# Performance work log

Measured on AMD Instinct MI355X. Metric: run time of the kernel, lower is better.

Reference implementation:

```python
import jax, jax.numpy as jnp
import numpy as np

C = 8      # num_channels
H = 512    # dim_hidden
B, S = 32, 1024
EPS = 1e-5


def _layernorm(x, gamma, beta):
    mu = jnp.mean(x, axis=-1, keepdims=True)
    var = jnp.var(x, axis=-1, keepdims=True)
    return (x - mu) * jax.lax.rsqrt(var + EPS) * gamma + beta


def setup_inputs() -> dict:
    key = jax.random.key(0)
    ks = jax.random.split(key, 7)
    x = jax.random.normal(ks[0], (C, B, S, 1), dtype=jnp.float32)
    # per-channel Linear(1,H): torch weight [H,1] -> stacked as [C,H]
    enc_w = jax.random.normal(ks[1], (C, H), dtype=jnp.float32) / jnp.sqrt(1.0)
    enc_b = jax.random.normal(ks[2], (C, H), dtype=jnp.float32) * 0.02
    enc_gamma = jnp.ones((C, H), dtype=jnp.float32)
    enc_beta = jnp.zeros((C, H), dtype=jnp.float32)
    # modulator Linear(C*H -> H): torch weight [H, C*H]
    mod_w = jax.random.normal(ks[3], (H, C * H), dtype=jnp.float32) / jnp.sqrt(C * H)
    mod_b = jax.random.normal(ks[4], (H,), dtype=jnp.float32) * 0.02
    mod_gamma = jnp.ones((H,), dtype=jnp.float32)
    mod_beta = jnp.zeros((H,), dtype=jnp.float32)
    return {
        "x": x,
        "enc_w": enc_w, "enc_b": enc_b,
        "enc_gamma": enc_gamma, "enc_beta": enc_beta,
        "mod_w": mod_w, "mod_b": mod_b,
        "mod_gamma": mod_gamma, "mod_beta": mod_beta,
    }


def reference(x, enc_w, enc_b, enc_gamma, enc_beta, mod_w, mod_b, mod_gamma, mod_beta):
    # per-channel Linear(1,H): h[c,b,s,:] = x[c,b,s,0]*enc_w[c] + enc_b[c]
    h = x * enc_w[:, None, None, :] + enc_b[:, None, None, :]      # [C,B,S,H]
    h = _layernorm(h, enc_gamma[:, None, None, :], enc_beta[:, None, None, :])
    h = jax.nn.gelu(h, approximate=False)
    # concat along last dim in channel order -> [B,S,C*H]
    h = jnp.transpose(h, (1, 2, 0, 3)).reshape(B, S, C * H)
    # channel modulator: Linear + LayerNorm + GELU
    y = jnp.einsum("bsk,hk->bsh", h, mod_w) + mod_b                # [B,S,H]
    y = _layernorm(y, mod_gamma, mod_beta)
    return jax.nn.gelu(y, approximate=False)
```

## Files before the change

kernel.cpp:

```cpp
#include <hip/hip_runtime.h>
#include <hip/hip_bf16.h>
#include <math.h>

#define C_CH 8
#define H_DIM 512
#define BS 32768
#define K_DIM 4096
#define EPS 1e-5f

#define TM 64
#define TK 32
#define NKT (K_DIM / TK)
#define TMTK (TM * TK)

typedef __bf16 bf16x8 __attribute__((ext_vector_type(8)));
typedef __bf16 bf16x4 __attribute__((ext_vector_type(4)));
typedef float  floatx4 __attribute__((ext_vector_type(4)));

__device__ __forceinline__ float gelu_fast(float v) {
    float x2 = v * fmaf(v * v, 0.102943215f, 2.30220815f);
    float e = __builtin_amdgcn_exp2f(-x2);
    return v * __builtin_amdgcn_rcpf(1.0f + e);
}

__global__ __launch_bounds__(256) void prep_kernel(
    const float* __restrict__ w, __bf16* __restrict__ o,
    const float* __restrict__ enc_w, const float* __restrict__ enc_b,
    const float* __restrict__ enc_gamma,
    float* __restrict__ Wf, float* __restrict__ Bf, float* __restrict__ st)
{
    __shared__ float red[4][5];
    if (blockIdx.x < 1024) {
        int gtid  = blockIdx.x * 256 + threadIdx.x;
        int lane  = gtid & 63;
        int chunk = gtid >> 6;
        int kt    = chunk >> 5;
        int ntile = chunk & 31;
        int col   = ntile * 16 + (lane & 15);
        int k     = kt * 32 + (lane >> 4) * 8;
        const float* src = w + (size_t)col * K_DIM + k;
        float4 a = *(const float4*)src;
        float4 b = *(const float4*)(src + 4);
        bf16x8 h;
        h[0] = (__bf16)a.x; h[1] = (__bf16)a.y; h[2] = (__bf16)a.z; h[3] = (__bf16)a.w;
        h[4] = (__bf16)b.x; h[5] = (__bf16)b.y; h[6] = (__bf16)b.z; h[7] = (__bf16)b.w;
        *(bf16x8*)(o + (size_t)gtid * 8) = h;
    } else {
        const int c = blockIdx.x - 1024;
        const int t = threadIdx.x;
        const float* wp = enc_w + c * H_DIM;
        const float* bp = enc_b + c * H_DIM;
        const float* gp = enc_gamma + c * H_DIM;
        float w0 = wp[t], w1 = wp[t + 256];
        float b0 = bp[t], b1 = bp[t + 256];
        float sw  = w0 + w1;
        float sb  = b0 + b1;
        float sww = fmaf(w0, w0, w1 * w1);
        float sbb = fmaf(b0, b0, b1 * b1);
        float swb = fmaf(w0, b0, w1 * b1);
        #pragma unroll
        for (int off = 32; off; off >>= 1) {
            sw  += __shfl_xor(sw,  off);
            sb  += __shfl_xor(sb,  off);
            sww += __shfl_xor(sww, off);
            sbb += __shfl_xor(sbb, off);
            swb += __shfl_xor(swb, off);
        }
        int wv = t >> 6, ln = t & 63;
        if (ln == 0) {
            red[wv][0] = sw;  red[wv][1] = sb;  red[wv][2] = sww;
            red[wv][3] = sbb; red[wv][4] = swb;
        }
        __syncthreads();
        float tsw  = red[0][0] + red[1][0] + red[2][0] + red[3][0];
        float tsb  = red[0][1] + red[1][1] + red[2][1] + red[3][1];
        float tsww = red[0][2] + red[1][2] + red[2][2] + red[3][2];
        float tsbb = red[0][3] + red[1][3] + red[2][3] + red[3][3];
        float tswb = red[0][4] + red[1][4] + red[2][4] + red[3][4];
        const float inv = 1.0f / (float)H_DIM;
        float mw = tsw * inv, mb = tsb * inv;
        if (t == 0) {
            st[c * 4 + 0] = tsww * inv - mw * mw;
            st[c * 4 + 1] = 2.0f * (tswb * inv - mw * mb);
            st[c * 4 + 2] = tsbb * inv - mb * mb;
        }
        float g0 = gp[t], g1 = gp[t + 256];
        Wf[c * H_DIM + t]       = g0 * (w0 - mw);
        Wf[c * H_DIM + t + 256] = g1 * (w1 - mw);
        Bf[c * H_DIM + t]       = g0 * (b0 - mb);
        Bf[c * H_DIM + t + 256] = g1 * (b1 - mb);
    }
}

template <int USE_WS>
__global__ __launch_bounds__(512, 4) void fused_gemm_kernel(
    const float* __restrict__ x,
    const float* __restrict__ enc_w,
    const float* __restrict__ enc_b,
    const float* __restrict__ enc_gamma,
    const float* __restrict__ enc_beta,
    const float* __restrict__ mod_w,
    const __bf16* __restrict__ Wb,
    const float* __restrict__ Wf,
    const float* __restrict__ Bf,
    const float* __restrict__ st,
    const float* __restrict__ mod_b,
    const float* __restrict__ mod_gamma,
    const float* __restrict__ mod_beta,
    float* __restrict__ out)
{
    __shared__ float stats[C_CH][5];
    __shared__ float pS[C_CH][TM];
    __shared__ float qS[C_CH][TM];
    __shared__ float rS[C_CH][TM];
    __shared__ __align__(16) __bf16 Als[2 * 4 * TMTK];
    __shared__ float redS[TM][8];
    __shared__ float redQ[TM][8];
    __shared__ float muS[TM];
    __shared__ float invS[TM];

    const int tid  = threadIdx.x;
    const int wave = tid >> 6;
    const int lane = tid & 63;
    const int row0 = blockIdx.x * TM;

    if (USE_WS) {
        int c = wave;
        int m = lane;
        float xv = x[c * BS + row0 + m];
        float vw = st[c * 4 + 0], cwb2 = st[c * 4 + 1], vb = st[c * 4 + 2];
        float q = rsqrtf(fmaf(xv, fmaf(xv, vw, cwb2), vb) + EPS);
        pS[c][m] = xv * q;
        qS[c][m] = q;
    } else {
        {
            const int c = wave;
            float sw = 0.f, sb = 0.f, sww = 0.f, sbb = 0.f, swb = 0.f;
            for (int j = lane; j < H_DIM; j += 64) {
                float w = enc_w[c * H_DIM + j];
                float b = enc_b[c * H_DIM + j];
                sw += w; sb += b;
                sww = fmaf(w, w, sww);
                sbb = fmaf(b, b, sbb);
                swb = fmaf(w, b, swb);
            }
            #pragma unroll
            for (int off = 32; off; off >>= 1) {
                sw  += __shfl_xor(sw,  off);
                sb  += __shfl_xor(sb,  off);
                sww += __shfl_xor(sww, off);
                sbb += __shfl_xor(sbb, off);
                swb += __shfl_xor(swb, off);
            }
            if (lane == 0) {
                const float inv = 1.0f / (float)H_DIM;
                float mw = sw * inv, mb = sb * inv;
                stats[c][0] = mw;
                stats[c][1] = mb;
                stats[c][2] = sww * inv - mw * mw;
                stats[c][3] = sbb * inv - mb * mb;
                stats[c][4] = swb * inv - mw * mb;
            }
        }
        __syncthreads();
        {
            int c = wave;
            int m = lane;
            float xv = x[c * BS + row0 + m];
            float mw = stats[c][0], mb = stats[c][1];
            float vw = stats[c][2], vb = stats[c][3], cwb = stats[c][4];
            float var = fmaf(xv, fmaf(xv, vw, 2.0f * cwb), vb);
            float q = rsqrtf(var + EPS);
            float p = xv * q;
            pS[c][m] = p;
            qS[c][m] = q;
            rS[c][m] = -fmaf(p, mw, q * mb);
        }
    }
    __syncthreads();

    const int wn = wave;
    const int lr = lane & 15;
    const int lq = lane >> 4;

    const int arow  = tid >> 3;
    const int akq   = (tid >> 1) & 3;
    const int ahalf = tid & 1;
    const int wchunk = arow * 4 + (akq ^ ((arow >> 1) & 3));

    floatx4 acc[4][4];
    #pragma unroll
    for (int i = 0; i < 4; ++i)
        #pragma unroll
        for (int j = 0; j < 4; ++j)
            acc[i][j] = (floatx4){0.f, 0.f, 0.f, 0.f};

    auto stageA2 = [&](int ktn, __bf16* dst, float p, float q) {
        const int j0 = ktn * TK + akq * 8 + ahalf * 4;
        float4 w = *(const float4*)(Wf + j0);
        float4 b = *(const float4*)(Bf + j0);
        float4 e = *(const float4*)(enc_beta + j0);
        float fw[4] = {w.x, w.y, w.z, w.w};
        float fb[4] = {b.x, b.y, b.z, b.w};
        float fe[4] = {e.x, e.y, e.z, e.w};
        bf16x4 hv;
        #pragma unroll
        for (int i = 0; i < 4; ++i) {
            float v = fmaf(p, fw[i], fmaf(q, fb[i], fe[i]));
            hv[i] = (__bf16)gelu_fast(v);
        }
        *(bf16x4*)(dst + wchunk * 8 + ahalf * 4) = hv;
    };

    auto stageA_legacy = [&](int ktn, __bf16* dst) {
        const int k0 = ktn * TK;
        const int c  = k0 >> 9;
        const int j0 = c * H_DIM + (k0 & (H_DIM - 1)) + akq * 8 + ahalf * 4;
        float p = pS[c][arow], q = qS[c][arow], r = rS[c][arow];
        float4 w = *(const float4*)(enc_w + j0);
        float4 b = *(const float4*)(enc_b + j0);
        float4 g = *(const float4*)(enc_gamma + j0);
        float4 e = *(const float4*)(enc_beta + j0);
        float fw[4] = {w.x, w.y, w.z, w.w};
        float fb[4] = {b.x, b.y, b.z, b.w};
        float fg[4] = {g.x, g.y, g.z, g.w};
        float fe[4] = {e.x, e.y, e.z, e.w};
        bf16x4 hv;
        #pragma unroll
        for (int i = 0; i < 4; ++i) {
            float t = fmaf(p, fw[i], fmaf(q, fb[i], r));
            float v = fmaf(t, fg[i], fe[i]);
            hv[i] = (__bf16)gelu_fast(v);
        }
        *(bf16x4*)(dst + wchunk * 8 + ahalf * 4) = hv;
    };

    const __bf16* baseB = Wb + ((size_t)(wn * 4) * 64 + lane) * 8;
    auto loadB = [&](int ktn, int half, bf16x8* dst) {
        if (USE_WS) {
            const __bf16* bp = baseB + ktn * 16384 + half * 1024;
            dst[0] = *(const bf16x8*)(bp);
            dst[1] = *(const bf16x8*)(bp + 512);
        } else {
            const int kk = ktn * 32 + lq * 8;
            #pragma unroll
            for (int nt = 0; nt < 2; ++nt) {
                int col = wn * 64 + (half * 2 + nt) * 16 + lr;
                const float* src = mod_w + (size_t)col * K_DIM + kk;
                float4 a = *(const float4*)src;
                float4 b = *(const float4*)(src + 4);
                bf16x8 h;
                h[0] = (__bf16)a.x; h[1] = (__bf16)a.y; h[2] = (__bf16)a.z; h[3] = (__bf16)a.w;
                h[4] = (__bf16)b.x; h[5] = (__bf16)b.y; h[6] = (__bf16)b.z; h[7] = (__bf16)b.w;
                dst[nt] = h;
            }
        }
    };

    bf16x8 bfrP[2], bfrQ[2];
    loadB(0, 0, bfrP);
    if (USE_WS) {
        float p0 = pS[0][arow], q0 = qS[0][arow];
        #pragma unroll
        for (int sub = 0; sub < 4; ++sub)
            stageA2(sub, Als + sub * TMTK, p0, q0);
    } else {
        #pragma unroll
        for (int sub = 0; sub < 4; ++sub)
            stageA_legacy(sub, Als + sub * TMTK);
    }
    __syncthreads();

    for (int g = 0; g < NKT / 4; ++g) {
        const __bf16* cur = Als + (g & 1) * (4 * TMTK);
        __bf16*       nxt = Als + ((g + 1) & 1) * (4 * TMTK);
        const bool haveNext = (g + 1 < NKT / 4);

        float pC = 0.f, qC = 0.f;
        if (USE_WS && haveNext) {
            const int cn = (g + 1) >> 2;
            pC = pS[cn][arow];
            qC = qS[cn][arow];
        }

        #pragma unroll
        for (int sub = 0; sub < 4; ++sub) {
            const int kt = g * 4 + sub;

            loadB(kt, 1, bfrQ);

            if (haveNext) {
                if (USE_WS) stageA2(kt + 4, nxt + sub * TMTK, pC, qC);
                else        stageA_legacy(kt + 4, nxt + sub * TMTK);
            }

            const __bf16* Acur = cur + sub * TMTK;
            bf16x8 af[4];
            #pragma unroll
            for (int mt = 0; mt < 4; ++mt) {
                int row = mt * 16 + lr;
                int chunk = row * 4 + (lq ^ ((row >> 1) & 3));
                af[mt] = *(const bf16x8*)(Acur + chunk * 8);
            }

            #pragma unroll
            for (int mt = 0; mt < 4; ++mt)
                #pragma unroll
                for (int nt = 0; nt < 2; ++nt)
                    acc[mt][nt] = __builtin_amdgcn_mfma_f32_16x16x32_bf16(
                        af[mt], bfrP[nt], acc[mt][nt], 0, 0, 0);

            if (kt + 1 < NKT) loadB(kt + 1, 0, bfrP);

            #pragma unroll
            for (int mt = 0; mt < 4; ++mt)
                #pragma unroll
                for (int nt = 0; nt < 2; ++nt)
                    acc[mt][nt + 2] = __builtin_amdgcn_mfma_f32_16x16x32_bf16(
                        af[mt], bfrQ[nt], acc[mt][nt + 2], 0, 0, 0);
        }
        __syncthreads();
    }

    float mbv[4], gv[4], bev[4];
    #pragma unroll
    for (int nt = 0; nt < 4; ++nt) {
        int col = wn * 64 + nt * 16 + lr;
        mbv[nt] = mod_b[col];
        gv[nt]  = mod_gamma[col];
        bev[nt] = mod_beta[col];
    }
    #pragma unroll
    for (int mt = 0; mt < 4; ++mt)
        #pragma unroll
        for (int nt = 0; nt < 4; ++nt)
            #pragma unroll
            for (int r = 0; r < 4; ++r)
                acc[mt][nt][r] += mbv[nt];

    #pragma unroll
    for (int mt = 0; mt < 4; ++mt) {
        #pragma unroll
        for (int r = 0; r < 4; ++r) {
            float s = 0.f, ss = 0.f;
            #pragma unroll
            for (int nt = 0; nt < 4; ++nt) {
                float y = acc[mt][nt][r];
                s += y;
                ss = fmaf(y, y, ss);
            }
            #pragma unroll
            for (int off = 1; off < 16; off <<= 1) {
                s  += __shfl_xor(s,  off);
                ss += __shfl_xor(ss, off);
            }
            if (lr == 0) {
                int row = mt * 16 + lq * 4 + r;
                redS[row][wn] = s;
                redQ[row][wn] = ss;
            }
        }
    }
    __syncthreads();
    if (tid < TM) {
        float s = 0.f, ss = 0.f;
        #pragma unroll
        for (int w = 0; w < 8; ++w) {
            s  += redS[tid][w];
            ss += redQ[tid][w];
        }
        const float inv_n = 1.0f / (float)H_DIM;
        float mu  = s * inv_n;
        float var = ss * inv_n - mu * mu;
        muS[tid]  = mu;
        invS[tid] = rsqrtf(var + EPS);
    }
    __syncthreads();

    #pragma unroll
    for (int mt = 0; mt < 4; ++mt) {
        #pragma unroll
        for (int r = 0; r < 4; ++r) {
            int row = mt * 16 + lq * 4 + r;
            float mu  = muS[row];
            float inv = invS[row];
            float* op = out + (size_t)(row0 + row) * H_DIM;
            #pragma unroll
            for (int nt = 0; nt < 4; ++nt) {
                int col = wn * 64 + nt * 16 + lr;
                float t = fmaf((acc[mt][nt][r] - mu) * inv, gv[nt], bev[nt]);
                op[col] = gelu_fast(t);
            }
        }
    }
}

extern "C" void kernel_launch(void* const* d_in, const int* in_sizes, int n_in,
                              void* d_out, int out_size, void* d_ws, size_t ws_size,
                              hipStream_t stream) {
    const float* x         = (const float*)d_in[0];
    const float* enc_w     = (const float*)d_in[1];
    const float* enc_b     = (const float*)d_in[2];
    const float* enc_gamma = (const float*)d_in[3];
    const float* enc_beta  = (const float*)d_in[4];
    const float* mod_w     = (const float*)d_in[5];
    const float* mod_b     = (const float*)d_in[6];
    const float* mod_gamma = (const float*)d_in[7];
    const float* mod_beta  = (const float*)d_in[8];
    float* out = (float*)d_out;

    const size_t wb_bytes = (size_t)H_DIM * K_DIM * sizeof(__bf16);
    const size_t wf_off   = wb_bytes;
    const size_t bf_off   = wf_off + (size_t)C_CH * H_DIM * sizeof(float);
    const size_t st_off   = bf_off + (size_t)C_CH * H_DIM * sizeof(float);
    const size_t need     = st_off + (size_t)C_CH * 4 * sizeof(float);

    int use_ws = (ws_size >= need) ? 1 : 0;
    __bf16* Wb = (__bf16*)d_ws;
    float*  Wf = (float*)((char*)d_ws + wf_off);
    float*  Bf = (float*)((char*)d_ws + bf_off);
    float*  st = (float*)((char*)d_ws + st_off);

    if (use_ws) {
        prep_kernel<<<1024 + C_CH, 256, 0, stream>>>(
            mod_w, Wb, enc_w, enc_b, enc_gamma, Wf, Bf, st);
        fused_gemm_kernel<1><<<BS / TM, 512, 0, stream>>>(
            x, enc_w, enc_b, enc_gamma, enc_beta, mod_w, Wb, Wf, Bf, st,
            mod_b, mod_gamma, mod_beta, out);
    } else {
        fused_gemm_kernel<0><<<BS / TM, 512, 0, stream>>>(
            x, enc_w, enc_b, enc_gamma, enc_beta, mod_w, Wb,
            (const float*)0, (const float*)0, (const float*)0,
            mod_b, mod_gamma, mod_beta, out);
    }
}
```

Measured before the change: 259.6 us.

## Switch GEMM to 32x32x16 MFMA with repacked weights and A staging

Replaces the 16x16x32 bf16 MFMA tiles with 32x32x16 MFMA, repacking the bf16 weight layout in the prep kernel and the shared-memory A tile layout to match. A staging now writes 8-element vectors, is spread over two slots per group, and drops the XOR swizzle. It also adds s_setprio around MFMA bursts. The aim is fewer MFMA and LDS instructions per FLOP and better overlap of GELU staging with matrix work, at the cost of a new epilogue row mapping and possible LDS bank conflicts without the swizzle.

```diff
diff --git a/kernel.cpp b/kernel.cpp
--- a/kernel.cpp
+++ b/kernel.cpp
@@ -11,11 +11,12 @@
 #define TM 64
 #define TK 32
 #define NKT (K_DIM / TK)
-#define TMTK (TM * TK)
+#define GRP 4
+#define NGRP (NKT / GRP)
+#define AELEMS (TM * TK * GRP)
 
 typedef __bf16 bf16x8 __attribute__((ext_vector_type(8)));
-typedef __bf16 bf16x4 __attribute__((ext_vector_type(4)));
-typedef float  floatx4 __attribute__((ext_vector_type(4)));
+typedef float  floatx16 __attribute__((ext_vector_type(16)));
 
 __device__ __forceinline__ float gelu_fast(float v) {
     float x2 = v * fmaf(v * v, 0.102943215f, 2.30220815f);
@@ -34,10 +35,10 @@
         int gtid  = blockIdx.x * 256 + threadIdx.x;
         int lane  = gtid & 63;
         int chunk = gtid >> 6;
-        int kt    = chunk >> 5;
-        int ntile = chunk & 31;
-        int col   = ntile * 16 + (lane & 15);
-        int k     = kt * 32 + (lane >> 4) * 8;
+        int kh    = chunk >> 4;
+        int n32   = chunk & 15;
+        int col   = n32 * 32 + (lane & 31);
+        int k     = kh * 16 + (lane >> 5) * 8;
         const float* src = w + (size_t)col * K_DIM + k;
         float4 a = *(const float4*)src;
         float4 b = *(const float4*)(src + 4);
@@ -113,7 +114,7 @@
     __shared__ float pS[C_CH][TM];
     __shared__ float qS[C_CH][TM];
     __shared__ float rS[C_CH][TM];
-    __shared__ __align__(16) __bf16 Als[2 * 4 * TMTK];
+    __shared__ __align__(16) __bf16 Als[2 * AELEMS];
     __shared__ float redS[TM][8];
     __shared__ float redQ[TM][8];
     __shared__ float muS[TM];
@@ -180,73 +181,85 @@
     __syncthreads();
 
     const int wn = wave;
-    const int lr = lane & 15;
-    const int lq = lane >> 4;
-
-    const int arow  = tid >> 3;
-    const int akq   = (tid >> 1) & 3;
-    const int ahalf = tid & 1;
-    const int wchunk = arow * 4 + (akq ^ ((arow >> 1) & 3));
-
-    floatx4 acc[4][4];
+
+    const int scg   = tid >> 6;
+    const int sq    = scg & 3;
+    const int skh   = sq >> 1;
+    const int smt   = sq & 1;
+    const int sl    = tid & 63;
+    const int skoff = skh * 16 + (sl >> 5) * 8;
+    const int arow  = smt * 32 + (sl & 31);
+    const int ssub0 = scg >> 2;
+    const int sdst0 = (sq * 512) + sl * 8;
+
+    floatx16 acc[2][2];
     #pragma unroll
-    for (int i = 0; i < 4; ++i)
-        #pragma unroll
-        for (int j = 0; j < 4; ++j)
-            acc[i][j] = (floatx4){0.f, 0.f, 0.f, 0.f};
-
-    auto stageA2 = [&](int ktn, __bf16* dst, float p, float q) {
-        const int j0 = ktn * TK + akq * 8 + ahalf * 4;
-        float4 w = *(const float4*)(Wf + j0);
-        float4 b = *(const float4*)(Bf + j0);
-        float4 e = *(const float4*)(enc_beta + j0);
-        float fw[4] = {w.x, w.y, w.z, w.w};
-        float fb[4] = {b.x, b.y, b.z, b.w};
-        float fe[4] = {e.x, e.y, e.z, e.w};
-        bf16x4 hv;
-        #pragma unroll
-        for (int i = 0; i < 4; ++i) {
+    for (int i = 0; i < 2; ++i)
+        #pragma unroll
+        for (int j = 0; j < 2; ++j)
+            #pragma unroll
+            for (int r = 0; r < 16; ++r)
+                acc[i][j][r] = 0.f;
+
+    auto stageSlot = [&](int g1, int which, __bf16* dstbuf, float p, float q) {
+        const int sub = ssub0 + which * 2;
+        const int k0  = (g1 * GRP + sub) * TK + skoff;
+        float4 w0 = *(const float4*)(Wf + k0);
+        float4 w1 = *(const float4*)(Wf + k0 + 4);
+        float4 b0 = *(const float4*)(Bf + k0);
+        float4 b1 = *(const float4*)(Bf + k0 + 4);
+        float4 e0 = *(const float4*)(enc_beta + k0);
+        float4 e1 = *(const float4*)(enc_beta + k0 + 4);
+        float fw[8] = {w0.x, w0.y, w0.z, w0.w, w1.x, w1.y, w1.z, w1.w};
+        float fb[8] = {b0.x, b0.y, b0.z, b0.w, b1.x, b1.y, b1.z, b1.w};
+        float fe[8] = {e0.x, e0.y, e0.z, e0.w, e1.x, e1.y, e1.z, e1.w};
+        bf16x8 hv;
+        #pragma unroll
+        for (int i = 0; i < 8; ++i) {
             float v = fmaf(p, fw[i], fmaf(q, fb[i], fe[i]));
             hv[i] = (__bf16)gelu_fast(v);
         }
-        *(bf16x4*)(dst + wchunk * 8 + ahalf * 4) = hv;
+        *(bf16x8*)(dstbuf + sub * 2048 + sdst0) = hv;
     };
 
-    auto stageA_legacy = [&](int ktn, __bf16* dst) {
-        const int k0 = ktn * TK;
-        const int c  = k0 >> 9;
-        const int j0 = c * H_DIM + (k0 & (H_DIM - 1)) + akq * 8 + ahalf * 4;
-        float p = pS[c][arow], q = qS[c][arow], r = rS[c][arow];
-        float4 w = *(const float4*)(enc_w + j0);
-        float4 b = *(const float4*)(enc_b + j0);
-        float4 g = *(const float4*)(enc_gamma + j0);
-        float4 e = *(const float4*)(enc_beta + j0);
-        float fw[4] = {w.x, w.y, w.z, w.w};
-        float fb[4] = {b.x, b.y, b.z, b.w};
-        float fg[4] = {g.x, g.y, g.z, g.w};
-        float fe[4] = {e.x, e.y, e.z, e.w};
-        bf16x4 hv;
-        #pragma unroll
-        for (int i = 0; i < 4; ++i) {
+    auto stageSlotL = [&](int g1, int which, __bf16* dstbuf,
+                          float p, float q, float r) {
+        const int sub = ssub0 + which * 2;
+        const int k0  = (g1 * GRP + sub) * TK + skoff;
+        float4 w0 = *(const float4*)(enc_w + k0);
+        float4 w1 = *(const float4*)(enc_w + k0 + 4);
+        float4 b0 = *(const float4*)(enc_b + k0);
+        float4 b1 = *(const float4*)(enc_b + k0 + 4);
+        float4 g0 = *(const float4*)(enc_gamma + k0);
+        float4 g1v = *(const float4*)(enc_gamma + k0 + 4);
+        float4 e0 = *(const float4*)(enc_beta + k0);
+        float4 e1 = *(const float4*)(enc_beta + k0 + 4);
+        float fw[8] = {w0.x, w0.y, w0.z, w0.w, w1.x, w1.y, w1.z, w1.w};
+        float fb[8] = {b0.x, b0.y, b0.z, b0.w, b1.x, b1.y, b1.z, b1.w};
+        float fg[8] = {g0.x, g0.y, g0.z, g0.w, g1v.x, g1v.y, g1v.z, g1v.w};
+        float fe[8] = {e0.x, e0.y, e0.z, e0.w, e1.x, e1.y, e1.z, e1.w};
+        bf16x8 hv;
+        #pragma unroll
+        for (int i = 0; i < 8; ++i) {
             float t = fmaf(p, fw[i], fmaf(q, fb[i], r));
             float v = fmaf(t, fg[i], fe[i]);
             hv[i] = (__bf16)gelu_fast(v);
         }
-        *(bf16x4*)(dst + wchunk * 8 + ahalf * 4) = hv;
+        *(bf16x8*)(dstbuf + sub * 2048 + sdst0) = hv;
     };
 
-    const __bf16* baseB = Wb + ((size_t)(wn * 4) * 64 + lane) * 8;
-    auto loadB = [&](int ktn, int half, bf16x8* dst) {
+    const __bf16* baseB = Wb + (size_t)(wn * 128 + lane) * 8;
+    auto loadB = [&](int kt, int half, bf16x8* dst) {
         if (USE_WS) {
-            const __bf16* bp = baseB + ktn * 16384 + half * 1024;
-            dst[0] = *(const bf16x8*)(bp);
+            const __bf16* bp = baseB + (size_t)(2 * kt + half) * 8192;
+            dst[0] = *(const bf16x8*)bp;
             dst[1] = *(const bf16x8*)(bp + 512);
         } else {
-            const int kk = ktn * 32 + lq * 8;
+            const int k = (2 * kt + half) * 16 + (lane >> 5) * 8;
             #pragma unroll
             for (int nt = 0; nt < 2; ++nt) {
-                int col = wn * 64 + (half * 2 + nt) * 16 + lr;
-                const float* src = mod_w + (size_t)col * K_DIM + kk;
+                int col = (wn * 2 + nt) * 32 + (lane & 31);
+                const float* src = mod_w + (size_t)col * K_DIM + k;
                 float4 a = *(const float4*)src;
                 float4 b = *(const float4*)(src + 4);
                 bf16x8 h;
@@ -261,101 +274,105 @@
     loadB(0, 0, bfrP);
     if (USE_WS) {
         float p0 = pS[0][arow], q0 = qS[0][arow];
-        #pragma unroll
-        for (int sub = 0; sub < 4; ++sub)
-            stageA2(sub, Als + sub * TMTK, p0, q0);
+        stageSlot(0, 0, Als, p0, q0);
+        stageSlot(0, 1, Als, p0, q0);
     } else {
-        #pragma unroll
-        for (int sub = 0; sub < 4; ++sub)
-            stageA_legacy(sub, Als + sub * TMTK);
+        float p0 = pS[0][arow], q0 = qS[0][arow], r0 = rS[0][arow];
+        stageSlotL(0, 0, Als, p0, q0, r0);
+        stageSlotL(0, 1, Als, p0, q0, r0);
     }
     __syncthreads();
 
-    for (int g = 0; g < NKT / 4; ++g) {
-        const __bf16* cur = Als + (g & 1) * (4 * TMTK);
-        __bf16*       nxt = Als + ((g + 1) & 1) * (4 * TMTK);
-        const bool haveNext = (g + 1 < NKT / 4);
-
-        float pC = 0.f, qC = 0.f;
-        if (USE_WS && haveNext) {
+    for (int g = 0; g < NGRP; ++g) {
+        __bf16* cur = Als + (g & 1) * AELEMS;
+        __bf16* nxt = Als + ((g + 1) & 1) * AELEMS;
+        const bool haveNext = (g + 1 < NGRP);
+
+        float pC = 0.f, qC = 0.f, rC = 0.f;
+        if (haveNext) {
             const int cn = (g + 1) >> 2;
             pC = pS[cn][arow];
             qC = qS[cn][arow];
-        }
-
-        #pragma unroll
-        for (int sub = 0; sub < 4; ++sub) {
-            const int kt = g * 4 + sub;
+            if (!USE_WS) rC = rS[cn][arow];
+        }
+
+        #pragma unroll
+        for (int sub = 0; sub < GRP; ++sub) {
+            const int kt = g * GRP + sub;
 
             loadB(kt, 1, bfrQ);
 
-            if (haveNext) {
-                if (USE_WS) stageA2(kt + 4, nxt + sub * TMTK, pC, qC);
-                else        stageA_legacy(kt + 4, nxt + sub * TMTK);
-            }
-
-            const __bf16* Acur = cur + sub * TMTK;
-            bf16x8 af[4];
-            #pragma unroll
-            for (int mt = 0; mt < 4; ++mt) {
-                int row = mt * 16 + lr;
-                int chunk = row * 4 + (lq ^ ((row >> 1) & 3));
-                af[mt] = *(const bf16x8*)(Acur + chunk * 8);
-            }
-
-            #pragma unroll
-            for (int mt = 0; mt < 4; ++mt)
+            if (haveNext && sub == 0) {
+                if (USE_WS) stageSlot(g + 1, 0, nxt, pC, qC);
+                else        stageSlotL(g + 1, 0, nxt, pC, qC, rC);
+            }
+            if (haveNext && sub == 2) {
+                if (USE_WS) stageSlot(g + 1, 1, nxt, pC, qC);
+                else        stageSlotL(g + 1, 1, nxt, pC, qC, rC);
+            }
+
+            const __bf16* Acur = cur + sub * (TM * TK);
+            bf16x8 af[2][2];
+            #pragma unroll
+            for (int kh = 0; kh < 2; ++kh)
+                #pragma unroll
+                for (int mt = 0; mt < 2; ++mt)
+                    af[kh][mt] = *(const bf16x8*)(Acur + (kh * 2 + mt) * 512 + lane * 8);
+
+            __builtin_amdgcn_s_setprio(1);
+            #pragma unroll
+            for (int mt = 0; mt < 2; ++mt)
                 #pragma unroll
                 for (int nt = 0; nt < 2; ++nt)
-                    acc[mt][nt] = __builtin_amdgcn_mfma_f32_16x16x32_bf16(
-                        af[mt], bfrP[nt], acc[mt][nt], 0, 0, 0);
+                    acc[mt][nt] = __builtin_amdgcn_mfma_f32_32x32x16_bf16(
+                        af[0][mt], bfrP[nt], acc[mt][nt], 0, 0, 0);
+            __builtin_amdgcn_s_setprio(0);
 
             if (kt + 1 < NKT) loadB(kt + 1, 0, bfrP);
 
-            #pragma unroll
-            for (int mt = 0; mt < 4; ++mt)
+            __builtin_amdgcn_s_setprio(1);
+            #pragma unroll
+            for (int mt = 0; mt < 2; ++mt)
                 #pragma unroll
                 for (int nt = 0; nt < 2; ++nt)
-                    acc[mt][nt + 2] = __builtin_amdgcn_mfma_f32_16x16x32_bf16(
-                        af[mt], bfrQ[nt], acc[mt][nt + 2], 0, 0, 0);
+                    acc[mt][nt] = __builtin_amdgcn_mfma_f32_32x32x16_bf16(
+                        af[1][mt], bfrQ[nt], acc[mt][nt], 0, 0, 0);
+            __builtin_amdgcn_s_setprio(0);
         }
         __syncthreads();
     }
 
-    float mbv[4], gv[4], bev[4];
+    float mbv[2], gv[2], bev[2];
     #pragma unroll
-    for (int nt = 0; nt < 4; ++nt) {
-        int col = wn * 64 + nt * 16 + lr;
+    for (int nt = 0; nt < 2; ++nt) {
+        int col = wn * 64 + nt * 32 + (lane & 31);
         mbv[nt] = mod_b[col];
         gv[nt]  = mod_gamma[col];
         bev[nt] = mod_beta[col];
     }
     #pragma unroll
-    for (int mt = 0; mt < 4; ++mt)
-        #pragma unroll
-        for (int nt = 0; nt < 4; ++nt)
-            #pragma unroll
-            for (int r = 0; r < 4; ++r)
+    for (int mt = 0; mt < 2; ++mt)
+        #pragma unroll
+        for (int nt = 0; nt < 2; ++nt)
+            #pragma unroll
+            for (int r = 0; r < 16; ++r)
                 acc[mt][nt][r] += mbv[nt];
 
     #pragma unroll
-    for (int mt = 0; mt < 4; ++mt) {
-        #pragma unroll
-        for (int r = 0; r < 4; ++r) {
-            float s = 0.f, ss = 0.f;
-            #pragma unroll
-            for (int nt = 0; nt < 4; ++nt) {
-                float y = acc[mt][nt][r];
-                s += y;
-                ss = fmaf(y, y, ss);
-            }
-            #pragma unroll
-            for (int off = 1; off < 16; off <<= 1) {
+    for (int mt = 0; mt < 2; ++mt) {
+        #pragma unroll
+        for (int r = 0; r < 16; ++r) {
+            float y0 = acc[mt][0][r];
+            float y1 = acc[mt][1][r];
+            float s  = y0 + y1;
+            float ss = fmaf(y0, y0, y1 * y1);
+            #pragma unroll
+            for (int off = 1; off < 32; off <<= 1) {
                 s  += __shfl_xor(s,  off);
                 ss += __shfl_xor(ss, off);
             }
-            if (lr == 0) {
-                int row = mt * 16 + lq * 4 + r;
+            if ((lane & 31) == 0) {
+                int row = mt * 32 + (r & 3) + ((r >> 2) << 3) + ((lane >> 5) << 2);
                 redS[row][wn] = s;
                 redQ[row][wn] = ss;
             }
@@ -378,16 +395,16 @@
     __syncthreads();
 
     #pragma unroll
-    for (int mt = 0; mt < 4; ++mt) {
-        #pragma unroll
-        for (int r = 0; r < 4; ++r) {
-            int row = mt * 16 + lq * 4 + r;
+    for (int mt = 0; mt < 2; ++mt) {
+        #pragma unroll
+        for (int r = 0; r < 16; ++r) {
+            int row = mt * 32 + (r & 3) + ((r >> 2) << 3) + ((lane >> 5) << 2);
             float mu  = muS[row];
             float inv = invS[row];
             float* op = out + (size_t)(row0 + row) * H_DIM;
             #pragma unroll
-            for (int nt = 0; nt < 4; ++nt) {
-                int col = wn * 64 + nt * 16 + lr;
+            for (int nt = 0; nt < 2; ++nt) {
+                int col = wn * 64 + nt * 32 + (lane & 31);
                 float t = fmaf((acc[mt][nt][r] - mu) * inv, gv[nt], bev[nt]);
                 op[col] = gelu_fast(t);
             }
```

New measurement: 270.0 us. 1.04x slower.

## Stage B tiles into LDS via async global_load_lds with double-buffered pipeline

Applied to the files above, without the earlier changes.

The bf16 weight tiles now go straight from global memory into double-buffered LDS using global_load_lds, where before each wave loaded them into registers. Next-next A-operand parameters are prefetched, and the GELU-encoded A tile is computed for step k+1 while the MFMAs of step k run. Each k-step has a single barrier, and s_setprio is raised around the MFMA clusters. The aim is to hide weight-load latency and cut register pressure, at the cost of about 78KB of dynamic LDS per block. That LDS footprint lowers occupancy below the launch-bound target of 4 blocks.

```diff
diff --git a/kernel.cpp b/kernel.cpp
--- a/kernel.cpp
+++ b/kernel.cpp
@@ -11,16 +11,28 @@
 #define TM 64
 #define TK 32
 #define NKT (K_DIM / TK)
-#define TMTK (TM * TK)
 
 typedef __bf16 bf16x8 __attribute__((ext_vector_type(8)));
 typedef __bf16 bf16x4 __attribute__((ext_vector_type(4)));
 typedef float  floatx4 __attribute__((ext_vector_type(4)));
+
+#define SMEM_BLS 0
+#define SMEM_ALS 65536
+#define SMEM_PS  73728
+#define SMEM_QS  75776
+#define SMEM_ST  77824
+#define SMEM_SZ  78080
 
 __device__ __forceinline__ float gelu_fast(float v) {
     float x2 = v * fmaf(v * v, 0.102943215f, 2.30220815f);
     float e = __builtin_amdgcn_exp2f(-x2);
     return v * __builtin_amdgcn_rcpf(1.0f + e);
+}
+
+__device__ __forceinline__ void gld_lds16(const void* g, void* l) {
+    __builtin_amdgcn_global_load_lds(
+        (const __attribute__((address_space(1))) void*)g,
+        (__attribute__((address_space(3))) void*)l, 16, 0, 0);
 }
 
 __global__ __launch_bounds__(256) void prep_kernel(
@@ -109,36 +121,40 @@
     const float* __restrict__ mod_beta,
     float* __restrict__ out)
 {
-    __shared__ float stats[C_CH][5];
-    __shared__ float pS[C_CH][TM];
-    __shared__ float qS[C_CH][TM];
-    __shared__ float rS[C_CH][TM];
-    __shared__ __align__(16) __bf16 Als[2 * 4 * TMTK];
-    __shared__ float redS[TM][8];
-    __shared__ float redQ[TM][8];
-    __shared__ float muS[TM];
-    __shared__ float invS[TM];
+    extern __shared__ __align__(16) char smem[];
+    float* pSf = (float*)(smem + SMEM_PS);
+    float* qSf = (float*)(smem + SMEM_QS);
+    float* statsF = (float*)(smem + SMEM_ST);
+    float* rSf = (float*)(smem + SMEM_BLS + 8192);
 
     const int tid  = threadIdx.x;
     const int wave = tid >> 6;
     const int lane = tid & 63;
+    const int lr   = lane & 15;
+    const int lq   = lane >> 4;
     const int row0 = blockIdx.x * TM;
 
+    const int smt   = tid >> 7;
+    const int ssl   = (tid >> 1) & 63;
+    const int shalf = tid & 1;
+    const int srow  = smt * 16 + (ssl & 15);
+    const int skoff = (ssl >> 4) * 8 + shalf * 4;
+    const int sdoff = smt * 1024 + ssl * 16 + shalf * 8;
+
     if (USE_WS) {
-        int c = wave;
-        int m = lane;
+        int c = wave, m = lane;
         float xv = x[c * BS + row0 + m];
         float vw = st[c * 4 + 0], cwb2 = st[c * 4 + 1], vb = st[c * 4 + 2];
         float q = rsqrtf(fmaf(xv, fmaf(xv, vw, cwb2), vb) + EPS);
-        pS[c][m] = xv * q;
-        qS[c][m] = q;
+        pSf[c * TM + m] = xv * q;
+        qSf[c * TM + m] = q;
     } else {
         {
             const int c = wave;
             float sw = 0.f, sb = 0.f, sww = 0.f, sbb = 0.f, swb = 0.f;
-            for (int j = lane; j < H_DIM; j += 64) {
-                float w = enc_w[c * H_DIM + j];
-                float b = enc_b[c * H_DIM + j];
+            for (int jj = lane; jj < H_DIM; jj += 64) {
+                float w = enc_w[c * H_DIM + jj];
+                float b = enc_b[c * H_DIM + jj];
                 sw += w; sb += b;
                 sww = fmaf(w, w, sww);
                 sbb = fmaf(b, b, sbb);
@@ -155,38 +171,28 @@
             if (lane == 0) {
                 const float inv = 1.0f / (float)H_DIM;
                 float mw = sw * inv, mb = sb * inv;
-                stats[c][0] = mw;
-                stats[c][1] = mb;
-                stats[c][2] = sww * inv - mw * mw;
-                stats[c][3] = sbb * inv - mb * mb;
-                stats[c][4] = swb * inv - mw * mb;
+                statsF[c * 5 + 0] = mw;
+                statsF[c * 5 + 1] = mb;
+                statsF[c * 5 + 2] = sww * inv - mw * mw;
+                statsF[c * 5 + 3] = sbb * inv - mb * mb;
+                statsF[c * 5 + 4] = swb * inv - mw * mb;
             }
         }
         __syncthreads();
         {
-            int c = wave;
-            int m = lane;
+            int c = wave, m = lane;
             float xv = x[c * BS + row0 + m];
-            float mw = stats[c][0], mb = stats[c][1];
-            float vw = stats[c][2], vb = stats[c][3], cwb = stats[c][4];
+            float mw = statsF[c * 5 + 0], mb = statsF[c * 5 + 1];
+            float vw = statsF[c * 5 + 2], vb = statsF[c * 5 + 3], cwb = statsF[c * 5 + 4];
             float var = fmaf(xv, fmaf(xv, vw, 2.0f * cwb), vb);
             float q = rsqrtf(var + EPS);
             float p = xv * q;
-            pS[c][m] = p;
-            qS[c][m] = q;
-            rS[c][m] = -fmaf(p, mw, q * mb);
+            pSf[c * TM + m] = p;
+            qSf[c * TM + m] = q;
+            rSf[c * TM + m] = -fmaf(p, mw, q * mb);
         }
     }
     __syncthreads();
-
-    const int wn = wave;
-    const int lr = lane & 15;
-    const int lq = lane >> 4;
-
-    const int arow  = tid >> 3;
-    const int akq   = (tid >> 1) & 3;
-    const int ahalf = tid & 1;
-    const int wchunk = arow * 4 + (akq ^ ((arow >> 1) & 3));
 
     floatx4 acc[4][4];
     #pragma unroll
@@ -195,11 +201,18 @@
         for (int j = 0; j < 4; ++j)
             acc[i][j] = (floatx4){0.f, 0.f, 0.f, 0.f};
 
-    auto stageA2 = [&](int ktn, __bf16* dst, float p, float q) {
-        const int j0 = ktn * TK + akq * 8 + ahalf * 4;
-        float4 w = *(const float4*)(Wf + j0);
-        float4 b = *(const float4*)(Bf + j0);
-        float4 e = *(const float4*)(enc_beta + j0);
+    auto stageB = [&](int j) {
+        const int r = j & 1;
+        #pragma unroll
+        for (int nt = 0; nt < 4; ++nt) {
+            const int chunk = j * 32 + wave * 4 + nt;
+            const char* g = (const char*)Wb + (size_t)chunk * 1024 + lane * 16;
+            void* l = smem + SMEM_BLS + r * 32768 + (wave * 4 + nt) * 1024;
+            gld_lds16(g, l);
+        }
+    };
+
+    auto computeA = [&](int j, float4 w, float4 b, float4 e, float p, float q) {
         float fw[4] = {w.x, w.y, w.z, w.w};
         float fb[4] = {b.x, b.y, b.z, b.w};
         float fe[4] = {e.x, e.y, e.z, e.w};
@@ -209,123 +222,154 @@
             float v = fmaf(p, fw[i], fmaf(q, fb[i], fe[i]));
             hv[i] = (__bf16)gelu_fast(v);
         }
-        *(bf16x4*)(dst + wchunk * 8 + ahalf * 4) = hv;
+        *(bf16x4*)(smem + SMEM_ALS + (j & 1) * 4096 + sdoff) = hv;
     };
 
-    auto stageA_legacy = [&](int ktn, __bf16* dst) {
-        const int k0 = ktn * TK;
-        const int c  = k0 >> 9;
-        const int j0 = c * H_DIM + (k0 & (H_DIM - 1)) + akq * 8 + ahalf * 4;
-        float p = pS[c][arow], q = qS[c][arow], r = rS[c][arow];
-        float4 w = *(const float4*)(enc_w + j0);
-        float4 b = *(const float4*)(enc_b + j0);
-        float4 g = *(const float4*)(enc_gamma + j0);
-        float4 e = *(const float4*)(enc_beta + j0);
-        float fw[4] = {w.x, w.y, w.z, w.w};
-        float fb[4] = {b.x, b.y, b.z, b.w};
-        float fg[4] = {g.x, g.y, g.z, g.w};
-        float fe[4] = {e.x, e.y, e.z, e.w};
-        bf16x4 hv;
-        #pragma unroll
-        for (int i = 0; i < 4; ++i) {
-            float t = fmaf(p, fw[i], fmaf(q, fb[i], r));
-            float v = fmaf(t, fg[i], fe[i]);
-            hv[i] = (__bf16)gelu_fast(v);
-        }
-        *(bf16x4*)(dst + wchunk * 8 + ahalf * 4) = hv;
+    auto mfmaPhase = [&](int kt) {
+        const __bf16* Ab = (const __bf16*)(smem + SMEM_ALS + (kt & 1) * 4096);
+        const char*   Bb = smem + SMEM_BLS + (kt & 1) * 32768 + wave * 4096;
+        bf16x8 af0 = *(const bf16x8*)(Ab + 0 * 512 + lane * 8);
+        bf16x8 af1 = *(const bf16x8*)(Ab + 1 * 512 + lane * 8);
+        bf16x8 af2 = *(const bf16x8*)(Ab + 2 * 512 + lane * 8);
+        bf16x8 af3 = *(const bf16x8*)(Ab + 3 * 512 + lane * 8);
+        bf16x8 b0 = *(const bf16x8*)(Bb + 0 * 1024 + lane * 16);
+        bf16x8 b1 = *(const bf16x8*)(Bb + 1 * 1024 + lane * 16);
+        __builtin_amdgcn_s_setprio(1);
+        acc[0][0] = __builtin_amdgcn_mfma_f32_16x16x32_bf16(af0, b0, acc[0][0], 0, 0, 0);
+        acc[1][0] = __builtin_amdgcn_mfma_f32_16x16x32_bf16(af1, b0, acc[1][0], 0, 0, 0);
+        acc[2][0] = __builtin_amdgcn_mfma_f32_16x16x32_bf16(af2, b0, acc[2][0], 0, 0, 0);
+        acc[3][0] = __builtin_amdgcn_mfma_f32_16x16x32_bf16(af3, b0, acc[3][0], 0, 0, 0);
+        acc[0][1] = __builtin_amdgcn_mfma_f32_16x16x32_bf16(af0, b1, acc[0][1], 0, 0, 0);
+        acc[1][1] = __builtin_amdgcn_mfma_f32_16x16x32_bf16(af1, b1, acc[1][1], 0, 0, 0);
+        acc[2][1] = __builtin_amdgcn_mfma_f32_16x16x32_bf16(af2, b1, acc[2][1], 0, 0, 0);
+        acc[3][1] = __builtin_amdgcn_mfma_f32_16x16x32_bf16(af3, b1, acc[3][1], 0, 0, 0);
+        __builtin_amdgcn_s_setprio(0);
+        b0 = *(const bf16x8*)(Bb + 2 * 1024 + lane * 16);
+        b1 = *(const bf16x8*)(Bb + 3 * 1024 + lane * 16);
+        __builtin_amdgcn_s_setprio(1);
+        acc[0][2] = __builtin_amdgcn_mfma_f32_16x16x32_bf16(af0, b0, acc[0][2], 0, 0, 0);
+        acc[1][2] = __builtin_amdgcn_mfma_f32_16x16x32_bf16(af1, b0, acc[1][2], 0, 0, 0);
+        acc[2][2] = __builtin_amdgcn_mfma_f32_16x16x32_bf16(af2, b0, acc[2][2], 0, 0, 0);
+        acc[3][2] = __builtin_amdgcn_mfma_f32_16x16x32_bf16(af3, b0, acc[3][2], 0, 0, 0);
+        acc[0][3] = __builtin_amdgcn_mfma_f32_16x16x32_bf16(af0, b1, acc[0][3], 0, 0, 0);
+        acc[1][3] = __builtin_amdgcn_mfma_f32_16x16x32_bf16(af1, b1, acc[1][3], 0, 0, 0);
+        acc[2][3] = __builtin_amdgcn_mfma_f32_16x16x32_bf16(af2, b1, acc[2][3], 0, 0, 0);
+        acc[3][3] = __builtin_amdgcn_mfma_f32_16x16x32_bf16(af3, b1, acc[3][3], 0, 0, 0);
+        __builtin_amdgcn_s_setprio(0);
     };
 
-    const __bf16* baseB = Wb + ((size_t)(wn * 4) * 64 + lane) * 8;
-    auto loadB = [&](int ktn, int half, bf16x8* dst) {
-        if (USE_WS) {
-            const __bf16* bp = baseB + ktn * 16384 + half * 1024;
-            dst[0] = *(const bf16x8*)(bp);
-            dst[1] = *(const bf16x8*)(bp + 512);
-        } else {
-            const int kk = ktn * 32 + lq * 8;
-            #pragma unroll
-            for (int nt = 0; nt < 2; ++nt) {
-                int col = wn * 64 + (half * 2 + nt) * 16 + lr;
-                const float* src = mod_w + (size_t)col * K_DIM + kk;
-                float4 a = *(const float4*)src;
-                float4 b = *(const float4*)(src + 4);
-                bf16x8 h;
-                h[0] = (__bf16)a.x; h[1] = (__bf16)a.y; h[2] = (__bf16)a.z; h[3] = (__bf16)a.w;
-                h[4] = (__bf16)b.x; h[5] = (__bf16)b.y; h[6] = (__bf16)b.z; h[7] = (__bf16)b.w;
-                dst[nt] = h;
-            }
-        }
-    };
-
-    bf16x8 bfrP[2], bfrQ[2];
-    loadB(0, 0, bfrP);
     if (USE_WS) {
-        float p0 = pS[0][arow], q0 = qS[0][arow];
-        #pragma unroll
-        for (int sub = 0; sub < 4; ++sub)
-            stageA2(sub, Als + sub * TMTK, p0, q0);
+        float pCur = pSf[srow];
+        float qCur = qSf[srow];
+        float4 paW, paB, paE, pbW, pbB, pbE;
+
+        stageB(0);
+        asm volatile("" ::: "memory");
+        paW = *(const float4*)(Wf + skoff);
+        paB = *(const float4*)(Bf + skoff);
+        paE = *(const float4*)(enc_beta + skoff);
+        asm volatile("" ::: "memory");
+        computeA(0, paW, paB, paE, pCur, qCur);
+        pbW = *(const float4*)(Wf + TK + skoff);
+        pbB = *(const float4*)(Bf + TK + skoff);
+        pbE = *(const float4*)(enc_beta + TK + skoff);
+        asm volatile("s_waitcnt lgkmcnt(0)" ::: "memory");
+        __builtin_amdgcn_s_barrier();
+        __builtin_amdgcn_sched_barrier(0);
+
+        auto fiter = [&](int kt, float4& cw, float4& cb, float4& ce,
+                         float4& nw, float4& nb, float4& ne) {
+            if (kt + 1 < NKT) stageB(kt + 1);
+            asm volatile("" ::: "memory");
+            if (kt + 2 < NKT) {
+                nw = *(const float4*)(Wf + (kt + 2) * TK + skoff);
+                nb = *(const float4*)(Bf + (kt + 2) * TK + skoff);
+                ne = *(const float4*)(enc_beta + (kt + 2) * TK + skoff);
+            }
+            asm volatile("" ::: "memory");
+            if (kt + 1 < NKT) {
+                if (((kt + 1) & 15) == 0) {
+                    pCur = pSf[((kt + 1) >> 4) * TM + srow];
+                    qCur = qSf[((kt + 1) >> 4) * TM + srow];
+                }
+                computeA(kt + 1, cw, cb, ce, pCur, qCur);
+            }
+            asm volatile("" ::: "memory");
+            if (kt == NKT - 1)
+                asm volatile("s_waitcnt vmcnt(0)" ::: "memory");
+            mfmaPhase(kt);
+            asm volatile("s_waitcnt lgkmcnt(0)" ::: "memory");
+            __builtin_amdgcn_s_barrier();
+            __builtin_amdgcn_sched_barrier(0);
+        };
+
+        for (int kt = 0; kt < NKT; kt += 2) {
+            fiter(kt,     pbW, pbB, pbE, paW, paB, paE);
+            fiter(kt + 1, paW, paB, paE, pbW, pbB, pbE);
+        }
     } else {
-        #pragma unroll
-        for (int sub = 0; sub < 4; ++sub)
-            stageA_legacy(sub, Als + sub * TMTK);
-    }
+        for (int kt = 0; kt < NKT; ++kt) {
+            {
+                int c = kt >> 4;
+                float p = pSf[c * TM + srow], q = qSf[c * TM + srow], r = rSf[c * TM + srow];
+                int k0 = kt * TK + skoff;
+                float4 w = *(const float4*)(enc_w + k0);
+                float4 b = *(const float4*)(enc_b + k0);
+                float4 g = *(const float4*)(enc_gamma + k0);
+                float4 e = *(const float4*)(enc_beta + k0);
+                float fw[4] = {w.x, w.y, w.z, w.w};
+                float fb[4] = {b.x, b.y, b.z, b.w};
+                float fg[4] = {g.x, g.y, g.z, g.w};
+                float fe[4] = {e.x, e.y, e.z, e.w};
+                bf16x4 hv;
+                #pragma unroll
+                for (int i = 0; i < 4; ++i) {
+                    float t = fmaf(p, fw[i], fmaf(q, fb[i], r));
+                    float v = fmaf(t, fg[i], fe[i]);
+                    hv[i] = (__bf16)gelu_fast(v);
+                }
+                *(bf16x4*)(smem + SMEM_ALS + sdoff) = hv;
+            }
+            __syncthreads();
+            {
+                const __bf16* Ab = (const __bf16*)(smem + SMEM_ALS);
+                bf16x8 af[4];
+                #pragma unroll
+                for (int mt = 0; mt < 4; ++mt)
+                    af[mt] = *(const bf16x8*)(Ab + mt * 512 + lane * 8);
+                #pragma unroll
+                for (int nt = 0; nt < 4; ++nt) {
+                    int col = wave * 64 + nt * 16 + lr;
+                    int kk  = kt * 32 + lq * 8;
+                    const float* src = mod_w + (size_t)col * K_DIM + kk;
+                    float4 a = *(const float4*)src;
+                    float4 b2 = *(const float4*)(src + 4);
+                    bf16x8 bb;
+                    bb[0] = (__bf16)a.x;  bb[1] = (__bf16)a.y;
+                    bb[2] = (__bf16)a.z;  bb[3] = (__bf16)a.w;
+                    bb[4] = (__bf16)b2.x; bb[5] = (__bf16)b2.y;
+                    bb[6] = (__bf16)b2.z; bb[7] = (__bf16)b2.w;
+                    #pragma unroll
+                    for (int mt = 0; mt < 4; ++mt)
+                        acc[mt][nt] = __builtin_amdgcn_mfma_f32_16x16x32_bf16(
+                            af[mt], bb, acc[mt][nt], 0, 0, 0);
+                }
+            }
+            __syncthreads();
+        }
+    }
+
+    asm volatile("s_waitcnt vmcnt(0) lgkmcnt(0)" ::: "memory");
     __syncthreads();
-
-    for (int g = 0; g < NKT / 4; ++g) {
-        const __bf16* cur = Als + (g & 1) * (4 * TMTK);
-        __bf16*       nxt = Als + ((g + 1) & 1) * (4 * TMTK);
-        const bool haveNext = (g + 1 < NKT / 4);
-
-        float pC = 0.f, qC = 0.f;
-        if (USE_WS && haveNext) {
-            const int cn = (g + 1) >> 2;
-            pC = pS[cn][arow];
-            qC = qS[cn][arow];
-        }
-
-        #pragma unroll
-        for (int sub = 0; sub < 4; ++sub) {
-            const int kt = g * 4 + sub;
-
-            loadB(kt, 1, bfrQ);
-
-            if (haveNext) {
-                if (USE_WS) stageA2(kt + 4, nxt + sub * TMTK, pC, qC);
-                else        stageA_legacy(kt + 4, nxt + sub * TMTK);
-            }
-
-            const __bf16* Acur = cur + sub * TMTK;
-            bf16x8 af[4];
-            #pragma unroll
-            for (int mt = 0; mt < 4; ++mt) {
-                int row = mt * 16 + lr;
-                int chunk = row * 4 + (lq ^ ((row >> 1) & 3));
-                af[mt] = *(const bf16x8*)(Acur + chunk * 8);
-            }
-
-            #pragma unroll
-            for (int mt = 0; mt < 4; ++mt)
-                #pragma unroll
-                for (int nt = 0; nt < 2; ++nt)
-                    acc[mt][nt] = __builtin_amdgcn_mfma_f32_16x16x32_bf16(
-                        af[mt], bfrP[nt], acc[mt][nt], 0, 0, 0);
-
-            if (kt + 1 < NKT) loadB(kt + 1, 0, bfrP);
-
-            #pragma unroll
-            for (int mt = 0; mt < 4; ++mt)
-                #pragma unroll
-                for (int nt = 0; nt < 2; ++nt)
-                    acc[mt][nt + 2] = __builtin_amdgcn_mfma_f32_16x16x32_bf16(
-                        af[mt], bfrQ[nt], acc[mt][nt + 2], 0, 0, 0);
-        }
-        __syncthreads();
-    }
+    float* redS = (float*)(smem + SMEM_BLS);
+    float* redQ = (float*)(smem + SMEM_BLS + 2048);
+    float* muS  = (float*)(smem + SMEM_BLS + 4096);
+    float* invS = (float*)(smem + SMEM_BLS + 4352);
 
     float mbv[4], gv[4], bev[4];
     #pragma unroll
     for (int nt = 0; nt < 4; ++nt) {
-        int col = wn * 64 + nt * 16 + lr;
+        int col = wave * 64 + nt * 16 + lr;
         mbv[nt] = mod_b[col];
         gv[nt]  = mod_gamma[col];
         bev[nt] = mod_beta[col];
@@ -356,8 +400,8 @@
             }
             if (lr == 0) {
                 int row = mt * 16 + lq * 4 + r;
-                redS[row][wn] = s;
-                redQ[row][wn] = ss;
+                redS[row * 8 + wave] = s;
+                redQ[row * 8 + wave] = ss;
             }
         }
     }
@@ -366,8 +410,8 @@
         float s = 0.f, ss = 0.f;
         #pragma unroll
         for (int w = 0; w < 8; ++w) {
-            s  += redS[tid][w];
-            ss += redQ[tid][w];
+            s  += redS[tid * 8 + w];
+            ss += redQ[tid * 8 + w];
         }
         const float inv_n = 1.0f / (float)H_DIM;
         float mu  = s * inv_n;
@@ -387,7 +431,7 @@
             float* op = out + (size_t)(row0 + row) * H_DIM;
             #pragma unroll
             for (int nt = 0; nt < 4; ++nt) {
-                int col = wn * 64 + nt * 16 + lr;
+                int col = wave * 64 + nt * 16 + lr;
                 float t = fmaf((acc[mt][nt][r] - mu) * inv, gv[nt], bev[nt]);
                 op[col] = gelu_fast(t);
             }
@@ -421,14 +465,23 @@
     float*  Bf = (float*)((char*)d_ws + bf_off);
     float*  st = (float*)((char*)d_ws + st_off);
 
+    static int attr_done = 0;
+    if (!attr_done) {
+        hipFuncSetAttribute((const void*)fused_gemm_kernel<1>,
+                            hipFuncAttributeMaxDynamicSharedMemorySize, SMEM_SZ);
+        hipFuncSetAttribute((const void*)fused_gemm_kernel<0>,
+                            hipFuncAttributeMaxDynamicSharedMemorySize, SMEM_SZ);
+        attr_done = 1;
+    }
+
     if (use_ws) {
         prep_kernel<<<1024 + C_CH, 256, 0, stream>>>(
             mod_w, Wb, enc_w, enc_b, enc_gamma, Wf, Bf, st);
-        fused_gemm_kernel<1><<<BS / TM, 512, 0, stream>>>(
+        fused_gemm_kernel<1><<<BS / TM, 512, SMEM_SZ, stream>>>(
             x, enc_w, enc_b, enc_gamma, enc_beta, mod_w, Wb, Wf, Bf, st,
             mod_b, mod_gamma, mod_beta, out);
     } else {
-        fused_gemm_kernel<0><<<BS / TM, 512, 0, stream>>>(
+        fused_gemm_kernel<0><<<BS / TM, 512, SMEM_SZ, stream>>>(
             x, enc_w, enc_b, enc_gamma, enc_beta, mod_w, Wb,
             (const float*)0, (const float*)0, (const float*)0,
             mod_b, mod_gamma, mod_beta, out);
```

Result: slower. 488.1 us (+88.0%).
